# Performance work log

Measured on AMD Instinct MI355X. Metric: run time of the kernel, lower is better.

Reference implementation:

```python
import jax, jax.numpy as jnp
import numpy as np

EMBED_DIM = 768
NUM_HEADS = 12
HEAD_DIM = EMBED_DIM // NUM_HEADS
MAX_WAVELENGTH = 10000.0
ROPE_PERCENT = 0.5


def p_rope(x, positions):
    """Partial RoPE (Gemma-style half-split layout) on x: [BH, S, D]."""
    rope_angles = int(ROPE_PERCENT * HEAD_DIM) // 2
    nope_angles = HEAD_DIM // 2 - rope_angles
    fraction = 2.0 * jnp.arange(rope_angles, dtype=x.dtype) / HEAD_DIM
    timescale = MAX_WAVELENGTH ** fraction
    # infinite timescale => angle 0 => identity rotation for the non-roped dims
    timescale = jnp.concatenate([timescale, jnp.full((nope_angles,), jnp.inf, dtype=x.dtype)])
    sinusoid = positions[:, None] / timescale[None, :]  # [S, D/2]
    sin, cos = jnp.sin(sinusoid), jnp.cos(sinusoid)
    x1, x2 = jnp.split(x, 2, axis=-1)  # each [BH, S, D/2]
    return jnp.concatenate([x1 * cos - x2 * sin, x2 * cos + x1 * sin], axis=-1)


def setup_inputs() -> dict:
    key = jax.random.key(0)
    ks = jax.random.split(key, 9)
    B, T, E = 16, 1024, EMBED_DIM
    s = 0.02
    return {
        "hidden_states": jax.random.normal(ks[0], (B, T, E), jnp.float32),
        "wq": jax.random.normal(ks[1], (E, E), jnp.float32) * s,
        "bq": jax.random.normal(ks[2], (E,), jnp.float32) * s,
        "wk": jax.random.normal(ks[3], (E, E), jnp.float32) * s,
        "bk": jax.random.normal(ks[4], (E,), jnp.float32) * s,
        "wv": jax.random.normal(ks[5], (E, E), jnp.float32) * s,
        "bv": jax.random.normal(ks[6], (E,), jnp.float32) * s,
        "wo": jax.random.normal(ks[7], (E, E), jnp.float32) * s,
        "bo": jax.random.normal(ks[8], (E,), jnp.float32) * s,
    }


def _shape(x, B, S):
    # [B, S, E] -> [B*H, S, head_dim]
    return x.reshape(B, S, NUM_HEADS, HEAD_DIM).transpose(0, 2, 1, 3).reshape(B * NUM_HEADS, S, HEAD_DIM)


def reference(hidden_states, wq, bq, wk, bk, wv, bv, wo, bo):
    B, T, E = hidden_states.shape
    scaling = HEAD_DIM ** -0.5
    # torch nn.Linear: y = x @ W.T + b
    q = (hidden_states @ wq.T + bq) * scaling
    k = hidden_states @ wk.T + bk
    v = hidden_states @ wv.T + bv
    q = _shape(q, B, T)  # [BH, T, D]
    k = _shape(k, B, T)
    v = _shape(v, B, T)
    positions = jnp.arange(T, dtype=hidden_states.dtype)
    k = p_rope(k, positions)
    q = p_rope(q, positions)
    attn = jnp.einsum('bqd,bkd->bqk', q, k)  # [BH, T, T]
    attn = jax.nn.softmax(attn, axis=-1)
    out = jnp.einsum('bqk,bkd->bqd', attn, v)  # [BH, T, D]
    out = out.reshape(B, NUM_HEADS, T, HEAD_DIM).transpose(0, 2, 1, 3).reshape(B, T, E)
    return out @ wo.T + bo
```

## Files before the change

kernel.cpp:

```cpp
#include <hip/hip_runtime.h>
#include <hip/hip_bf16.h>
#include <math.h>

typedef __hip_bfloat16 bf16;
typedef __attribute__((ext_vector_type(8))) __bf16 bf16x8;
typedef __attribute__((ext_vector_type(8))) unsigned short u16x8;
typedef __attribute__((ext_vector_type(4))) float f32x4;
typedef __attribute__((ext_vector_type(16))) float f32x16;
typedef unsigned int u32;
typedef __attribute__((ext_vector_type(4))) unsigned int u32x4;

#define DEVI static __device__ __forceinline__

#define BATCH 16
#define SEQ 1024
#define EMB 768
#define NHEAD 12
#define HDIM 64
#define BHEADS (BATCH * NHEAD)
#define MROWS (BATCH * SEQ)

DEVI f32x4 mfma16x16(bf16x8 a, bf16x8 b, f32x4 c) {
  return __builtin_amdgcn_mfma_f32_16x16x32_bf16(a, b, c, 0, 0, 0);
}
DEVI f32x16 mfma32x32(bf16x8 a, bf16x8 b, f32x16 c) {
  return __builtin_amdgcn_mfma_f32_32x32x16_bf16(a, b, c, 0, 0, 0);
}

DEVI void gload_lds16(const bf16* g, void* lds) {
  __builtin_amdgcn_global_load_lds(
      (const __attribute__((address_space(1))) void*)g,
      (__attribute__((address_space(3))) void*)lds, 16, 0, 0);
}

#if __has_builtin(__builtin_amdgcn_exp2f)
DEVI float fexp2(float x) { return __builtin_amdgcn_exp2f(x); }
#else
DEVI float fexp2(float x) { return exp2f(x); }
#endif

DEVI unsigned short f2bf_bits(float f) {
  bf16 h = __float2bfloat16(f);
  return *reinterpret_cast<unsigned short*>(&h);
}
DEVI u32 pack2(float lo, float hi) {
  return (u32)f2bf_bits(lo) | ((u32)f2bf_bits(hi) << 16);
}

__global__ __launch_bounds__(256) void convert_bf16_kernel(
    const float* __restrict__ src, bf16* __restrict__ dst, int n8) {
  int i = blockIdx.x * 256 + threadIdx.x;
  if (i >= n8) return;
  const float4* s = (const float4*)src + (long)i * 2;
  float4 a = s[0], b = s[1];
  u16x8 r;
  r[0] = f2bf_bits(a.x); r[1] = f2bf_bits(a.y);
  r[2] = f2bf_bits(a.z); r[3] = f2bf_bits(a.w);
  r[4] = f2bf_bits(b.x); r[5] = f2bf_bits(b.y);
  r[6] = f2bf_bits(b.z); r[7] = f2bf_bits(b.w);
  *(u16x8*)(dst + (long)i * 8) = r;
}

__global__ void rope_table_kernel(float2* __restrict__ tbl) {
  int i = blockIdx.x * 256 + threadIdx.x;
  if (i >= SEQ * 16) return;
  int t = i >> 4;
  int d = i & 15;
  double inv_ts = pow(10000.0, -(double)d / 32.0);
  double ang = (double)t * inv_ts;
  tbl[i] = make_float2((float)cos(ang), (float)sin(ang));
}

DEVI void gemm_core_768(const bf16* __restrict__ A, const bf16* __restrict__ Bt,
                        int rowBase, int colBase, bf16* Asm, bf16* Bsm,
                        f32x4 (&acc)[4][4]) {
  const int K = 768;
  const int tid = threadIdx.x;
  const int wave = tid >> 6;
  const int lane = tid & 63;
  const int c0 = lane & 15;
  const int khi = lane >> 4;
  const int wm = wave >> 1, wn = wave & 1;
  const int srow = tid >> 2;
  const int scol = (tid & 3) * 8;
  const bf16* aG = A + (long)(rowBase + srow) * K + scol;
  const bf16* bG = Bt + (long)(colBase + srow) * K + scol;
  char* aL0 = (char*)Asm + wave * 1024;
  char* aL1 = (char*)Asm + 4096 + wave * 1024;
  char* bL0 = (char*)Bsm + wave * 1024;
  char* bL1 = (char*)Bsm + 4096 + wave * 1024;
  const int stride64 = 64 * K;

  for (int kk = 0; kk < K; kk += 32) {
    gload_lds16(aG + kk, aL0);
    gload_lds16(aG + stride64 + kk, aL1);
    gload_lds16(bG + kk, bL0);
    gload_lds16(bG + stride64 + kk, bL1);
    asm volatile("s_waitcnt vmcnt(0)" ::: "memory");
    __syncthreads();
    bf16x8 af[4], bfr[4];
#pragma unroll
    for (int m = 0; m < 4; ++m)
      af[m] = *(const bf16x8*)(Asm + (wm * 64 + m * 16 + c0) * 32 + khi * 8);
#pragma unroll
    for (int n = 0; n < 4; ++n)
      bfr[n] = *(const bf16x8*)(Bsm + (wn * 64 + n * 16 + c0) * 32 + khi * 8);
#pragma unroll
    for (int m = 0; m < 4; ++m)
#pragma unroll
      for (int n = 0; n < 4; ++n)
        acc[m][n] = mfma16x16(af[m], bfr[n], acc[m][n]);
    __syncthreads();
  }
}

__global__ __launch_bounds__(256) void qkv_kernel(
    const bf16* __restrict__ hs,
    const bf16* __restrict__ wq, const float* __restrict__ bq,
    const bf16* __restrict__ wk, const float* __restrict__ bk,
    const bf16* __restrict__ wv, const float* __restrict__ bv,
    const float2* __restrict__ tbl,
    bf16* __restrict__ Qb, bf16* __restrict__ Kb, bf16* __restrict__ Vtb) {
  __shared__ __align__(16) bf16 Asm[128 * 32];
  __shared__ __align__(16) bf16 Bsm[128 * 32];
  const int type = blockIdx.z;
  const bf16* W = (type == 0) ? wq : (type == 1) ? wk : wv;
  const float* bias = (type == 0) ? bq : (type == 1) ? bk : bv;
  const int rowBase = blockIdx.x * 128;
  const int colBase = blockIdx.y * 128;
  f32x4 acc[4][4] = {};
  gemm_core_768(hs, W, rowBase, colBase, Asm, Bsm, acc);

  const int tid = threadIdx.x;
  const int wave = tid >> 6, lane = tid & 63;
  const int c0 = lane & 15, khi = lane >> 4;
  const int wm = wave >> 1, wn = wave & 1;
  const int colW = colBase + wn * 64;
  const int head = colW >> 6;
  float bb[4];
#pragma unroll
  for (int n = 0; n < 4; ++n) bb[n] = bias[colW + n * 16 + c0];

  const int rW = rowBase + wm * 64;
  const int bIdx = rW >> 10;
  const int bh = bIdx * NHEAD + head;

  if (type == 2) {
#pragma unroll
    for (int m = 0; m < 4; ++m) {
      const int t0 = (rW & 1023) + m * 16 + khi * 4;
#pragma unroll
      for (int n = 0; n < 4; ++n) {
        const int d = n * 16 + c0;
        bf16* vp = Vtb + ((long)bh * HDIM + d) * SEQ + t0;
        ushort4 pk;
        pk.x = f2bf_bits(acc[m][n][0] + bb[n]);
        pk.y = f2bf_bits(acc[m][n][1] + bb[n]);
        pk.z = f2bf_bits(acc[m][n][2] + bb[n]);
        pk.w = f2bf_bits(acc[m][n][3] + bb[n]);
        *(ushort4*)vp = pk;
      }
    }
  } else {
    const float scl = (type == 0) ? 0.125f * 1.44269504f : 1.0f;
    bf16* base = ((type == 0) ? Qb : Kb) + (long)bh * SEQ * HDIM;
#pragma unroll
    for (int m = 0; m < 4; ++m) {
#pragma unroll
      for (int ri = 0; ri < 4; ++ri) {
        const int t = (rW & 1023) + m * 16 + khi * 4 + ri;
        float v0 = (acc[m][0][ri] + bb[0]) * scl;
        float v1 = (acc[m][1][ri] + bb[1]) * scl;
        float v2 = (acc[m][2][ri] + bb[2]) * scl;
        float v3 = (acc[m][3][ri] + bb[3]) * scl;
        const float2 cs = tbl[t * 16 + c0];
        const float r0 = v0 * cs.x - v2 * cs.y;
        const float r2 = v2 * cs.x + v0 * cs.y;
        bf16* qp = base + (long)t * HDIM;
        qp[c0] = __float2bfloat16(r0);
        qp[16 + c0] = __float2bfloat16(v1);
        qp[32 + c0] = __float2bfloat16(r2);
        qp[48 + c0] = __float2bfloat16(v3);
      }
    }
  }
}


DEVI int swoff(int row, int s) {
  return row * 128 + (((s ^ (row & 7)) & 7) << 4);
}

__global__ __launch_bounds__(256, 2) void attn_kernel(
    const bf16* __restrict__ Q, const bf16* __restrict__ K,
    const bf16* __restrict__ Vt, bf16* __restrict__ Ao) {
  __shared__ __align__(16) char smem[4 * 8192];
  const int bid = blockIdx.x;
  const int xcd = bid & 7, idx = bid >> 3;
  const int bh = xcd + ((idx >> 2) << 3);
  const int qt = idx & 3;

  const int tid = threadIdx.x;
  const int lane = tid & 63;
  const int w = tid >> 6;
  const int l31 = lane & 31;
  const int hi = lane >> 5;

  const bf16* Qh = Q + (long)bh * SEQ * HDIM;
  const bf16* Kh = K + (long)bh * SEQ * HDIM;
  const bf16* Vh = Vt + (long)bh * HDIM * SEQ;

  const int qbase = qt * 256 + w * 64;
  bf16x8 qf[2][4];
#pragma unroll
  for (int qn = 0; qn < 2; ++qn)
#pragma unroll
    for (int ks = 0; ks < 4; ++ks)
      qf[qn][ks] = *(const bf16x8*)(Qh + (qbase + qn * 32 + l31) * HDIM +
                                    ks * 16 + hi * 8);

  f32x16 o[2][2] = {};
  float lacc[2] = {0.f, 0.f};

  const int sr = tid >> 3;
  const int sc = tid & 7;

  bf16x8 kr0 = *(const bf16x8*)(Kh + sr * HDIM + sc * 8);
  bf16x8 kr1 = *(const bf16x8*)(Kh + (sr + 32) * HDIM + sc * 8);
  bf16x8 vr0 = *(const bf16x8*)(Vh + sr * SEQ + sc * 8);
  bf16x8 vr1 = *(const bf16x8*)(Vh + (sr + 32) * SEQ + sc * 8);
  *(bf16x8*)(smem + swoff(sr, sc)) = kr0;
  *(bf16x8*)(smem + swoff(sr + 32, sc)) = kr1;
  *(bf16x8*)(smem + 16384 + swoff(sr, sc)) = vr0;
  *(bf16x8*)(smem + 16384 + swoff(sr + 32, sc)) = vr1;
  __syncthreads();

  for (int ct = 0; ct < SEQ / 64; ++ct) {
    const int co = (ct & 1) * 8192;
    const char* Kc = smem + co;
    const char* Vc = smem + 16384 + co;

    if (ct != 15) {
      const int nt = (ct + 1) * 64;
      kr0 = *(const bf16x8*)(Kh + (nt + sr) * HDIM + sc * 8);
      kr1 = *(const bf16x8*)(Kh + (nt + sr + 32) * HDIM + sc * 8);
      vr0 = *(const bf16x8*)(Vh + sr * SEQ + nt + sc * 8);
      vr1 = *(const bf16x8*)(Vh + (sr + 32) * SEQ + nt + sc * 8);
    }

    f32x16 s[2][2] = {};
#pragma unroll
    for (int m = 0; m < 2; ++m)
#pragma unroll
      for (int ks = 0; ks < 4; ++ks) {
        bf16x8 ka = *(const bf16x8*)(Kc + swoff(m * 32 + l31, ks * 2 + hi));
        s[m][0] = mfma32x32(ka, qf[0][ks], s[m][0]);
        s[m][1] = mfma32x32(ka, qf[1][ks], s[m][1]);
      }

    bf16x8 pf[2][4];
#pragma unroll
    for (int qn = 0; qn < 2; ++qn) {
      u32 wds[2][4][2];
#pragma unroll
      for (int m = 0; m < 2; ++m)
#pragma unroll
        for (int b = 0; b < 4; ++b)
#pragma unroll
          for (int pp = 0; pp < 2; ++pp) {
            const float p0 = fexp2(s[m][qn][4 * b + 2 * pp]);
            const float p1 = fexp2(s[m][qn][4 * b + 2 * pp + 1]);
            lacc[qn] += p0 + p1;
            wds[m][b][pp] = pack2(p0, p1);
          }
#pragma unroll
      for (int m = 0; m < 2; ++m)
#pragma unroll
        for (int ts = 0; ts < 2; ++ts) {
          u32 x0 = wds[m][2 * ts][0], y0 = wds[m][2 * ts + 1][0];
          u32 x1 = wds[m][2 * ts][1], y1 = wds[m][2 * ts + 1][1];
          asm("v_permlane32_swap_b32 %0, %1" : "+v"(x0), "+v"(y0));
          asm("v_permlane32_swap_b32 %0, %1" : "+v"(x1), "+v"(y1));
          u32x4 t = {x0, x1, y0, y1};
          pf[qn][2 * m + ts] = *(bf16x8*)&t;
        }
    }

#pragma unroll
    for (int dm = 0; dm < 2; ++dm)
#pragma unroll
      for (int tk = 0; tk < 4; ++tk) {
        bf16x8 va = *(const bf16x8*)(Vc + swoff(dm * 32 + l31, tk * 2 + hi));
        o[dm][0] = mfma32x32(va, pf[0][tk], o[dm][0]);
        o[dm][1] = mfma32x32(va, pf[1][tk], o[dm][1]);
      }

    if (ct != 15) {
      const int no = 8192 - co;
      *(bf16x8*)(smem + no + swoff(sr, sc)) = kr0;
      *(bf16x8*)(smem + no + swoff(sr + 32, sc)) = kr1;
      *(bf16x8*)(smem + 16384 + no + swoff(sr, sc)) = vr0;
      *(bf16x8*)(smem + 16384 + no + swoff(sr + 32, sc)) = vr1;
      __syncthreads();
    }
  }

#pragma unroll
  for (int qn = 0; qn < 2; ++qn) lacc[qn] += __shfl_xor(lacc[qn], 32);
  const float inv0 = 1.0f / lacc[0];
  const float inv1 = 1.0f / lacc[1];

  const int bb = bh / NHEAD;
  const int hh = bh % NHEAD;
#pragma unroll
  for (int qn = 0; qn < 2; ++qn) {
    const float inv = qn ? inv1 : inv0;
    const int t = qbase + qn * 32 + l31;
    bf16* orow = Ao + (long)(bb * SEQ + t) * EMB + hh * HDIM;
#pragma unroll
    for (int dm = 0; dm < 2; ++dm)
#pragma unroll
      for (int b = 0; b < 4; ++b)
#pragma unroll
        for (int pp = 0; pp < 2; ++pp) {
          const int r = 4 * b + 2 * pp;
          const int d = dm * 32 + 2 * pp + 8 * b + 4 * hi;
          *(u32*)(orow + d) = pack2(o[dm][qn][r] * inv, o[dm][qn][r + 1] * inv);
        }
  }
}

__global__ __launch_bounds__(256) void oproj_kernel(
    const bf16* __restrict__ X, const bf16* __restrict__ wo,
    const float* __restrict__ bo, float* __restrict__ out) {
  __shared__ __align__(16) bf16 Asm[128 * 32];
  __shared__ __align__(16) bf16 Bsm[128 * 32];
  const int rowBase = blockIdx.x * 128;
  const int colBase = blockIdx.y * 128;
  f32x4 acc[4][4] = {};
  gemm_core_768(X, wo, rowBase, colBase, Asm, Bsm, acc);
  const int tid = threadIdx.x;
  const int wave = tid >> 6, lane = tid & 63;
  const int c0 = lane & 15, khi = lane >> 4;
  const int wm = wave >> 1, wn = wave & 1;
  const int colW = colBase + wn * 64;
  float bb[4];
#pragma unroll
  for (int n = 0; n < 4; ++n) bb[n] = bo[colW + n * 16 + c0];
#pragma unroll
  for (int m = 0; m < 4; ++m)
#pragma unroll
    for (int ri = 0; ri < 4; ++ri) {
      const int row = rowBase + wm * 64 + m * 16 + khi * 4 + ri;
      float* op = out + (long)row * EMB + colW;
#pragma unroll
      for (int n = 0; n < 4; ++n)
        op[n * 16 + c0] = acc[m][n][ri] + bb[n];
    }
}

extern "C" void kernel_launch(void* const* d_in, const int* in_sizes, int n_in,
                              void* d_out, int out_size, void* d_ws, size_t ws_size,
                              hipStream_t stream) {
  const float* hs_f = (const float*)d_in[0];
  const float* wq_f = (const float*)d_in[1];
  const float* bq = (const float*)d_in[2];
  const float* wk_f = (const float*)d_in[3];
  const float* bk = (const float*)d_in[4];
  const float* wv_f = (const float*)d_in[5];
  const float* bv = (const float*)d_in[6];
  const float* wo_f = (const float*)d_in[7];
  const float* bo = (const float*)d_in[8];
  float* out = (float*)d_out;

  char* ws = (char*)d_ws;
  size_t off = 0;
  float2* tbl = (float2*)ws; off += 131072;
  const size_t hsBytes = (size_t)MROWS * EMB * 2;
  const size_t wBytes = (size_t)EMB * EMB * 2;
  const size_t bufBytes = (size_t)BHEADS * SEQ * HDIM * 2;
  bf16* hsb = (bf16*)(ws + off); off += hsBytes;
  bf16* wqb = (bf16*)(ws + off); off += wBytes;
  bf16* wkb = (bf16*)(ws + off); off += wBytes;
  bf16* wvb = (bf16*)(ws + off); off += wBytes;
  bf16* wob = (bf16*)(ws + off); off += wBytes;
  bf16* Qb = (bf16*)(ws + off); off += bufBytes;
  bf16* Kb = (bf16*)(ws + off); off += bufBytes;
  bf16* Vtb = (bf16*)(ws + off); off += bufBytes;
  bf16* Ao = (bf16*)(ws + off);

  const int nHs8 = MROWS * EMB / 8;
  const int nW8 = EMB * EMB / 8;
  convert_bf16_kernel<<<dim3(nHs8 / 256), dim3(256), 0, stream>>>(hs_f, hsb, nHs8);
  convert_bf16_kernel<<<dim3(nW8 / 256), dim3(256), 0, stream>>>(wq_f, wqb, nW8);
  convert_bf16_kernel<<<dim3(nW8 / 256), dim3(256), 0, stream>>>(wk_f, wkb, nW8);
  convert_bf16_kernel<<<dim3(nW8 / 256), dim3(256), 0, stream>>>(wv_f, wvb, nW8);
  convert_bf16_kernel<<<dim3(nW8 / 256), dim3(256), 0, stream>>>(wo_f, wob, nW8);
  rope_table_kernel<<<dim3(64), dim3(256), 0, stream>>>(tbl);
  qkv_kernel<<<dim3(MROWS / 128, EMB / 128, 3), dim3(256), 0, stream>>>(
      hsb, wqb, bq, wkb, bk, wvb, bv, tbl, Qb, Kb, Vtb);
  attn_kernel<<<dim3(768), dim3(256), 0, stream>>>(Qb, Kb, Vtb, Ao);
  oproj_kernel<<<dim3(MROWS / 128, EMB / 128), dim3(256), 0, stream>>>(Ao, wob, bo, out);
}
```

Baseline: 210.1 us.

## Double-buffer LDS tiles in shared GEMM core to overlap loads with MFMA

The 768-deep GEMM loop used by the QKV and output-projection kernels now keeps two LDS buffers. It prefetches the next 32-wide K slice with global-to-LDS loads while MFMAs run on the current slice, and the loop is unrolled by two to alternate between the buffers. The goal is to hide global memory latency that was previously exposed on every K step. In exchange, each block uses twice as much shared memory, which may lower occupancy.

```diff
diff --git a/kernel.cpp b/kernel.cpp
--- a/kernel.cpp
+++ b/kernel.cpp
@@ -91,27 +91,40 @@
   char* bL1 = (char*)Bsm + 4096 + wave * 1024;
   const int stride64 = 64 * K;
 
-  for (int kk = 0; kk < K; kk += 32) {
-    gload_lds16(aG + kk, aL0);
-    gload_lds16(aG + stride64 + kk, aL1);
-    gload_lds16(bG + kk, bL0);
-    gload_lds16(bG + stride64 + kk, bL1);
+#define G_STAGE(boff, kk)                                                    \
+  gload_lds16(aG + (kk), aL0 + (boff));                                      \
+  gload_lds16(aG + stride64 + (kk), aL1 + (boff));                           \
+  gload_lds16(bG + (kk), bL0 + (boff));                                      \
+  gload_lds16(bG + stride64 + (kk), bL1 + (boff));
+
+#define G_COMPUTE(be)                                                        \
+  {                                                                          \
+    bf16x8 af[4], bfr[4];                                                    \
+    _Pragma("unroll") for (int m = 0; m < 4; ++m) af[m] =                    \
+        *(const bf16x8*)(Asm + (be) + (wm * 64 + m * 16 + c0) * 32 + khi * 8); \
+    _Pragma("unroll") for (int n = 0; n < 4; ++n) bfr[n] =                   \
+        *(const bf16x8*)(Bsm + (be) + (wn * 64 + n * 16 + c0) * 32 + khi * 8); \
+    _Pragma("unroll") for (int m = 0; m < 4; ++m)                            \
+      _Pragma("unroll") for (int n = 0; n < 4; ++n)                          \
+        acc[m][n] = mfma16x16(af[m], bfr[n], acc[m][n]);                     \
+  }
+
+  G_STAGE(0, 0);
+  asm volatile("s_waitcnt vmcnt(0)" ::: "memory");
+  __syncthreads();
+
+  for (int kk = 0; kk < K; kk += 64) {
+    G_STAGE(8192, kk + 32);
+    G_COMPUTE(0);
     asm volatile("s_waitcnt vmcnt(0)" ::: "memory");
     __syncthreads();
-    bf16x8 af[4], bfr[4];
-#pragma unroll
-    for (int m = 0; m < 4; ++m)
-      af[m] = *(const bf16x8*)(Asm + (wm * 64 + m * 16 + c0) * 32 + khi * 8);
-#pragma unroll
-    for (int n = 0; n < 4; ++n)
-      bfr[n] = *(const bf16x8*)(Bsm + (wn * 64 + n * 16 + c0) * 32 + khi * 8);
-#pragma unroll
-    for (int m = 0; m < 4; ++m)
-#pragma unroll
-      for (int n = 0; n < 4; ++n)
-        acc[m][n] = mfma16x16(af[m], bfr[n], acc[m][n]);
+    if (kk + 64 < K) { G_STAGE(0, kk + 64); }
+    G_COMPUTE(4096);
+    asm volatile("s_waitcnt vmcnt(0)" ::: "memory");
     __syncthreads();
   }
+#undef G_STAGE
+#undef G_COMPUTE
 }
 
 __global__ __launch_bounds__(256) void qkv_kernel(
@@ -121,8 +134,8 @@
     const bf16* __restrict__ wv, const float* __restrict__ bv,
     const float2* __restrict__ tbl,
     bf16* __restrict__ Qb, bf16* __restrict__ Kb, bf16* __restrict__ Vtb) {
-  __shared__ __align__(16) bf16 Asm[128 * 32];
-  __shared__ __align__(16) bf16 Bsm[128 * 32];
+  __shared__ __align__(16) bf16 Asm[2 * 128 * 32];
+  __shared__ __align__(16) bf16 Bsm[2 * 128 * 32];
   const int type = blockIdx.z;
   const bf16* W = (type == 0) ? wq : (type == 1) ? wk : wv;
   const float* bias = (type == 0) ? bq : (type == 1) ? bk : bv;
@@ -333,8 +346,8 @@
 __global__ __launch_bounds__(256) void oproj_kernel(
     const bf16* __restrict__ X, const bf16* __restrict__ wo,
     const float* __restrict__ bo, float* __restrict__ out) {
-  __shared__ __align__(16) bf16 Asm[128 * 32];
-  __shared__ __align__(16) bf16 Bsm[128 * 32];
+  __shared__ __align__(16) bf16 Asm[2 * 128 * 32];
+  __shared__ __align__(16) bf16 Bsm[2 * 128 * 32];
   const int rowBase = blockIdx.x * 128;
   const int colBase = blockIdx.y * 128;
   f32x4 acc[4][4] = {};
```

Result: no change. 212.8 us (+1.3%).
